# Kernel tuning notes

Measured on AMD Instinct MI355X. Metric: run time of the kernel, lower is better.

Reference implementation:

```python
import jax, jax.numpy as jnp
import numpy as np

B, S, H = 2, 2048, 1024
NH = 16
HD = H // NH

def setup_inputs() -> dict:
    key = jax.random.key(0)
    ks = jax.random.split(key, 9)
    s = 1.0 / np.sqrt(H)
    return {
        "hidden_state": jax.random.normal(ks[0], (B, S, H), dtype=jnp.float32),
        "Wq": jax.random.normal(ks[1], (H, H), dtype=jnp.float32) * s,
        "bq": jnp.zeros((H,), dtype=jnp.float32),
        "Wk": jax.random.normal(ks[2], (H, H), dtype=jnp.float32) * s,
        "bk": jnp.zeros((H,), dtype=jnp.float32),
        "Wv": jax.random.normal(ks[3], (H, H), dtype=jnp.float32) * s,
        "bv": jnp.zeros((H,), dtype=jnp.float32),
        "Wo": jax.random.normal(ks[4], (H, H), dtype=jnp.float32) * s,
        "bo": jnp.zeros((H,), dtype=jnp.float32),
    }

def reference(hidden_state, Wq, bq, Wk, bk, Wv, bv, Wo, bo):
    x = hidden_state  # [B,S,H]
    def split(t):
        return t.reshape(B, S, NH, HD).transpose(0, 2, 1, 3)  # [B,NH,S,HD]
    q = split(x @ Wq.T + bq)
    k = split(x @ Wk.T + bk)
    v = split(x @ Wv.T + bv)
    scale = 1.0 / jnp.sqrt(jnp.asarray(HD, dtype=x.dtype))
    scores = jnp.einsum('bhqd,bhkd->bhqk', q, k) * scale  # [B,NH,S,S]
    probs = jax.nn.softmax(scores, axis=-1)
    out = jnp.einsum('bhqk,bhkd->bhqd', probs, v)  # [B,NH,S,HD]
    out = out.transpose(0, 2, 1, 3).reshape(B, S, H)
    return out @ Wo.T + bo
```

## Files before the change

### kernel.cpp

```cpp
#include <hip/hip_runtime.h>


#define BD 2
#define SD 2048
#define HDIM 1024
#define NHD 16
#define HDD 64
#define NTOK 4096
#define QSCALE 0.1803368801111204f

typedef float f32x4 __attribute__((ext_vector_type(4)));
typedef _Float16 f16x8 __attribute__((ext_vector_type(8)));
typedef _Float16 f16x4 __attribute__((ext_vector_type(4)));
typedef __fp16 fp16x2 __attribute__((ext_vector_type(2)));

__device__ __forceinline__ f32x4 mfma_f16(f16x8 a, f16x8 b, f32x4 c) {
  return __builtin_amdgcn_mfma_f32_16x16x32_f16(a, b, c, 0, 0, 0);
}

__device__ __forceinline__ unsigned int pk2h(float lo, float hi) {
  fp16x2 v = __builtin_amdgcn_cvt_pkrtz(lo, hi);
  return __builtin_bit_cast(unsigned int, v);
}

__global__ void convert_kernel(const float* __restrict__ x,
                               const float* __restrict__ wq, const float* __restrict__ wk,
                               const float* __restrict__ wv, const float* __restrict__ wo,
                               _Float16* __restrict__ dst) {
  const int total4 = (8 * 1024 * 1024) / 4;
  for (int idx = blockIdx.x * blockDim.x + threadIdx.x; idx < total4;
       idx += gridDim.x * blockDim.x) {
    int e = idx * 4;
    const float* s;
    if (e < 4 * 1024 * 1024) {
      s = x + e;
    } else {
      int w = (e - 4 * 1024 * 1024) >> 20;
      int off = e & 1048575;
      s = (w == 0 ? wq : w == 1 ? wk : w == 2 ? wv : wo) + off;
    }
    float4 v = *(const float4*)s;
    f16x4 h;
    h[0] = (_Float16)v.x; h[1] = (_Float16)v.y;
    h[2] = (_Float16)v.z; h[3] = (_Float16)v.w;
    *(f16x4*)(dst + e) = h;
  }
}

__device__ __forceinline__ void gemm_mainloop(
    const _Float16* __restrict__ Ap, const _Float16* __restrict__ Bp,
    int i0, int j0, _Float16* As, _Float16* Bs, f32x4 acc[4][4]) {
  const int tid = threadIdx.x;
  const int wid = tid >> 6, lane = tid & 63;
  const int lr = lane & 15, lg = lane >> 4;
  const int wm = wid >> 1, wn = wid & 1;
  const int srow = lane >> 2;
  const int scol = (lane & 3) * 8;

  for (int k0 = 0; k0 < HDIM; k0 += 32) {
#pragma unroll
    for (int it = 0; it < 2; ++it) {
      int rb = (wid * 2 + it) * 16;
      const _Float16* ga = Ap + (size_t)(i0 + rb + srow) * HDIM + k0 + scol;
      const _Float16* gb = Bp + (size_t)(j0 + rb + srow) * HDIM + k0 + scol;
      __builtin_amdgcn_global_load_lds(
          (__attribute__((address_space(1))) void*)ga,
          (__attribute__((address_space(3))) void*)(As + (wid * 2 + it) * 512), 16, 0, 0);
      __builtin_amdgcn_global_load_lds(
          (__attribute__((address_space(1))) void*)gb,
          (__attribute__((address_space(3))) void*)(Bs + (wid * 2 + it) * 512), 16, 0, 0);
    }
    __syncthreads();
    f16x8 af[4], bf[4];
#pragma unroll
    for (int mt = 0; mt < 4; mt++)
      af[mt] = *(const f16x8*)(As + (wm * 64 + mt * 16 + lr) * 32 + lg * 8);
#pragma unroll
    for (int nt = 0; nt < 4; nt++)
      bf[nt] = *(const f16x8*)(Bs + (wn * 64 + nt * 16 + lr) * 32 + lg * 8);
#pragma unroll
    for (int mt = 0; mt < 4; mt++)
#pragma unroll
      for (int nt = 0; nt < 4; nt++)
        acc[mt][nt] = mfma_f16(af[mt], bf[nt], acc[mt][nt]);
    __syncthreads();
  }
}

__global__ __launch_bounds__(256) void gemm_qkv(
    const _Float16* __restrict__ xb,
    const _Float16* __restrict__ wqb, const _Float16* __restrict__ wkb,
    const _Float16* __restrict__ wvb,
    const float* __restrict__ bq, const float* __restrict__ bk,
    const float* __restrict__ bv,
    _Float16* __restrict__ Qo, _Float16* __restrict__ Ko, _Float16* __restrict__ Vt) {
  __shared__ __attribute__((aligned(16))) _Float16 As[128 * 32];
  __shared__ __attribute__((aligned(16))) _Float16 Bs[128 * 32];
  const int bx = blockIdx.x;
  const int mat = bx >> 8;
  const int sub = bx & 255;
  const _Float16 *Ap, *Bp;
  int i0, j0;
  if (mat < 2) {
    Ap = xb; Bp = (mat ? wkb : wqb);
    i0 = (sub >> 3) * 128;
    j0 = (sub & 7) * 128;
  } else {
    Ap = wvb; Bp = xb;
    i0 = (sub & 7) * 128;
    j0 = (sub >> 3) * 128;
  }
  f32x4 acc[4][4];
#pragma unroll
  for (int a = 0; a < 4; a++)
#pragma unroll
    for (int b = 0; b < 4; b++) acc[a][b] = (f32x4){0.f, 0.f, 0.f, 0.f};

  gemm_mainloop(Ap, Bp, i0, j0, As, Bs, acc);

  const int tid = threadIdx.x;
  const int wid = tid >> 6, lane = tid & 63;
  const int lr = lane & 15, lg = lane >> 4;
  const int wm = wid >> 1, wn = wid & 1;
  const float* bias = (mat == 0 ? bq : mat == 1 ? bk : bv);

#pragma unroll
  for (int mt = 0; mt < 4; mt++) {
#pragma unroll
    for (int nt = 0; nt < 4; nt++) {
      int i = i0 + wm * 64 + mt * 16 + 4 * lg;
      int j = j0 + wn * 64 + nt * 16 + lr;
      if (mat < 2) {
        float bj = bias[j];
        int h = j >> 6, d = j & 63;
        _Float16* dst = (mat ? Ko : Qo);
        float scl = (mat == 0) ? QSCALE : 1.0f;
#pragma unroll
        for (int r = 0; r < 4; r++) {
          int tok = i + r;
          int b = tok >> 11, s = tok & 2047;
          dst[(((size_t)(b * NHD + h)) * SD + s) * HDD + d] =
              (_Float16)((acc[mt][nt][r] + bj) * scl);
        }
      } else {
        int tok = j;
        int b = tok >> 11, s = tok & 2047;
#pragma unroll
        for (int r = 0; r < 4; r++) {
          int wr = i + r;
          int h = wr >> 6, d = wr & 63;
          Vt[((size_t)(b * NHD + h) * HDD + d) * SD + s] =
              (_Float16)(acc[mt][nt][r] + bias[wr]);
        }
      }
    }
  }
}

__global__ __launch_bounds__(256) void gemm_out(
    const _Float16* __restrict__ attn, const _Float16* __restrict__ wob,
    const float* __restrict__ bo, float* __restrict__ out) {
  __shared__ __attribute__((aligned(16))) _Float16 As[128 * 32];
  __shared__ __attribute__((aligned(16))) _Float16 Bs[128 * 32];
  const int sub = blockIdx.x;
  const int i0 = (sub >> 3) * 128, j0 = (sub & 7) * 128;
  f32x4 acc[4][4];
#pragma unroll
  for (int a = 0; a < 4; a++)
#pragma unroll
    for (int b = 0; b < 4; b++) acc[a][b] = (f32x4){0.f, 0.f, 0.f, 0.f};

  gemm_mainloop(attn, wob, i0, j0, As, Bs, acc);

  const int tid = threadIdx.x;
  const int wid = tid >> 6, lane = tid & 63;
  const int lr = lane & 15, lg = lane >> 4;
  const int wm = wid >> 1, wn = wid & 1;
#pragma unroll
  for (int mt = 0; mt < 4; mt++) {
#pragma unroll
    for (int nt = 0; nt < 4; nt++) {
      int i = i0 + wm * 64 + mt * 16 + 4 * lg;
      int j = j0 + wn * 64 + nt * 16 + lr;
      float bj = bo[j];
#pragma unroll
      for (int r = 0; r < 4; r++)
        out[(size_t)(i + r) * HDIM + j] = acc[mt][nt][r] + bj;
    }
  }
}

__global__ __launch_bounds__(512) void attn_kernel(
    const _Float16* __restrict__ Q, const _Float16* __restrict__ K,
    const _Float16* __restrict__ VT, _Float16* __restrict__ AO) {
  const int g = blockIdx.x;
  const int xcd = g & 7, idx = g >> 3;
  const int qb = idx & 15;
  const int bh = xcd * 4 + (idx >> 4);
  const int tid = threadIdx.x, wv = tid >> 6, lane = tid & 63;
  const int lr = lane & 15, lg = lane >> 4;
  const int q0 = qb * 128 + wv * 16;
  const _Float16* Qh = Q + (size_t)bh * SD * HDD;
  const _Float16* Kh = K + (size_t)bh * SD * HDD;
  const _Float16* Vh = VT + (size_t)bh * HDD * SD;

  __shared__ __attribute__((aligned(16))) _Float16 Ks[2][2][64][32];
  __shared__ __attribute__((aligned(16))) _Float16 Vs[2][2][64][32];

  const int krow = lane >> 2;
  const int kswz = (((lane & 3) ^ ((lane >> 3) & 3)) * 8);
  const int kkf = wv & 1, krb = (wv >> 1) * 16;

  const int m  = lane & 15;
  const int u  = m & 3;
  const int sg = m >> 2;
  const int r4 = lane >> 4;
  const int c2 = (r4 >> 1) & 1;
  const int keyoff_e = 16 * (u >> 1) + 4 * (sg ^ c2)       + 2 * (u & 1);
  const int keyoff_o = 16 * (u >> 1) + 4 * (sg ^ (c2 | 2)) + 2 * (u & 1);
  const _Float16* Vrow[2];
  Vrow[0] = Vh + (size_t)(wv * 8 + 0 + r4) * SD + keyoff_e;
  Vrow[1] = Vh + (size_t)(wv * 8 + 4 + r4) * SD + keyoff_o;

  auto stage = [&](int b, int kv0) {
    const _Float16* gk = Kh + (size_t)(kv0 + krb + krow) * HDD + kkf * 32 + kswz;
    __builtin_amdgcn_global_load_lds(
        (__attribute__((address_space(1))) void*)gk,
        (__attribute__((address_space(3))) void*)(&Ks[b][kkf][krb][0]), 16, 0, 0);
#pragma unroll
    for (int kf = 0; kf < 2; kf++)
#pragma unroll
      for (int i = 0; i < 2; i++) {
        const _Float16* gv = Vrow[i] + kv0 + kf * 32;
        __builtin_amdgcn_global_load_lds(
            (__attribute__((address_space(1))) void*)gv,
            (__attribute__((address_space(3))) void*)(&Vs[b][kf][wv * 8 + i * 4][0]), 4, 0, 0);
      }
  };

  const int fswz = (lg ^ ((lr >> 1) & 3)) * 8;

  f16x8 qf[2];
#pragma unroll
  for (int kf = 0; kf < 2; kf++)
    qf[kf] = *(const f16x8*)(Qh + (size_t)(q0 + lr) * HDD + kf * 32 + lg * 8);

  f32x4 acc[4];
#pragma unroll
  for (int i = 0; i < 4; i++) acc[i] = (f32x4){0.f, 0.f, 0.f, 0.f};
  float mrun = -1e30f;
  float ls0 = 0.f, ls1 = 0.f, ls2 = 0.f, ls3 = 0.f;

  stage(0, 0);
  int cur = 0;

  for (int t = 0; t < SD / 64; ++t) {
    asm volatile("s_waitcnt vmcnt(0)" ::: "memory");
    __builtin_amdgcn_s_barrier();
    stage(cur ^ 1, ((t + 1) & (SD / 64 - 1)) * 64);

    f32x4 sc[4];
#pragma unroll
    for (int nt = 0; nt < 4; nt++) sc[nt] = (f32x4){0.f, 0.f, 0.f, 0.f};
    __builtin_amdgcn_s_setprio(1);
#pragma unroll
    for (int nt = 0; nt < 4; nt++)
#pragma unroll
      for (int kf = 0; kf < 2; kf++) {
        f16x8 kfr = *(const f16x8*)&Ks[cur][kf][nt * 16 + lr][fswz];
        sc[nt] = mfma_f16(kfr, qf[kf], sc[nt]);
      }
    __builtin_amdgcn_s_setprio(0);

    float t0 = fmaxf(fmaxf(sc[0][0], sc[0][1]), sc[0][2]);
    float t1 = fmaxf(fmaxf(sc[0][3], sc[1][0]), sc[1][1]);
    float t2 = fmaxf(fmaxf(sc[1][2], sc[1][3]), sc[2][0]);
    float t3 = fmaxf(fmaxf(sc[2][1], sc[2][2]), sc[2][3]);
    float t4 = fmaxf(fmaxf(sc[3][0], sc[3][1]), sc[3][2]);
    float tm = fmaxf(fmaxf(fmaxf(t0, t1), fmaxf(t2, t3)), fmaxf(t4, sc[3][3]));
    tm = fmaxf(tm, __shfl_xor(tm, 16));
    tm = fmaxf(tm, __shfl_xor(tm, 32));

    if (__any(tm - mrun > 8.0f)) {
      float mn = fmaxf(mrun, tm);
      float fm = exp2f(mrun - mn);
      mrun = mn;
      ls0 *= fm; ls1 *= fm; ls2 *= fm; ls3 *= fm;
#pragma unroll
      for (int ntd = 0; ntd < 4; ntd++)
#pragma unroll
        for (int r = 0; r < 4; r++) acc[ntd][r] *= fm;
    }

    {
      float p0[4], p1[4];
#pragma unroll
      for (int r = 0; r < 4; r++) p0[r] = exp2f(sc[0][r] - mrun);
#pragma unroll
      for (int r = 0; r < 4; r++) p1[r] = exp2f(sc[1][r] - mrun);
      ls0 += (p0[0] + p0[1]) + (p0[2] + p0[3]);
      ls1 += (p1[0] + p1[1]) + (p1[2] + p1[3]);
      unsigned int pw[4];
      pw[0] = pk2h(p0[0], p0[1]); pw[1] = pk2h(p0[2], p0[3]);
      pw[2] = pk2h(p1[0], p1[1]); pw[3] = pk2h(p1[2], p1[3]);
      f16x8 pb = __builtin_bit_cast(f16x8, *(unsigned int(*)[4])pw);
      __builtin_amdgcn_s_setprio(1);
#pragma unroll
      for (int ntd = 0; ntd < 4; ntd++) {
        f16x8 vf = *(const f16x8*)&Vs[cur][0][ntd * 16 + lr][fswz];
        acc[ntd] = mfma_f16(vf, pb, acc[ntd]);
      }
      __builtin_amdgcn_s_setprio(0);
    }
    {
      float p0[4], p1[4];
#pragma unroll
      for (int r = 0; r < 4; r++) p0[r] = exp2f(sc[2][r] - mrun);
#pragma unroll
      for (int r = 0; r < 4; r++) p1[r] = exp2f(sc[3][r] - mrun);
      ls2 += (p0[0] + p0[1]) + (p0[2] + p0[3]);
      ls3 += (p1[0] + p1[1]) + (p1[2] + p1[3]);
      unsigned int pw[4];
      pw[0] = pk2h(p0[0], p0[1]); pw[1] = pk2h(p0[2], p0[3]);
      pw[2] = pk2h(p1[0], p1[1]); pw[3] = pk2h(p1[2], p1[3]);
      f16x8 pb = __builtin_bit_cast(f16x8, *(unsigned int(*)[4])pw);
      __builtin_amdgcn_s_setprio(1);
#pragma unroll
      for (int ntd = 0; ntd < 4; ntd++) {
        f16x8 vf = *(const f16x8*)&Vs[cur][1][ntd * 16 + lr][fswz];
        acc[ntd] = mfma_f16(vf, pb, acc[ntd]);
      }
      __builtin_amdgcn_s_setprio(0);
    }
    cur ^= 1;
  }

  float lsum = (ls0 + ls1) + (ls2 + ls3);
  lsum += __shfl_xor(lsum, 16);
  lsum += __shfl_xor(lsum, 32);
  float inv = 1.0f / lsum;

  const int b = bh >> 4, h = bh & 15;
  _Float16* aoRow = AO + (size_t)(b * SD + q0 + lr) * HDIM + h * 64;
#pragma unroll
  for (int ntd = 0; ntd < 4; ntd++) {
    f16x4 o;
#pragma unroll
    for (int r = 0; r < 4; r++) o[r] = (_Float16)(acc[ntd][r] * inv);
    *(f16x4*)(aoRow + ntd * 16 + 4 * lg) = o;
  }
}

extern "C" void kernel_launch(void* const* d_in, const int* in_sizes, int n_in,
                              void* d_out, int out_size, void* d_ws, size_t ws_size,
                              hipStream_t stream) {
  const float* x  = (const float*)d_in[0];
  const float* Wq = (const float*)d_in[1];
  const float* bq = (const float*)d_in[2];
  const float* Wk = (const float*)d_in[3];
  const float* bk = (const float*)d_in[4];
  const float* Wv = (const float*)d_in[5];
  const float* bv = (const float*)d_in[6];
  const float* Wo = (const float*)d_in[7];
  const float* bo = (const float*)d_in[8];
  float* out = (float*)d_out;

  _Float16* xb  = (_Float16*)d_ws;
  _Float16* wqb = xb + 4 * 1024 * 1024;
  _Float16* wkb = wqb + 1024 * 1024;
  _Float16* wvb = wkb + 1024 * 1024;
  _Float16* wob = wvb + 1024 * 1024;
  _Float16* Qb  = wob + 1024 * 1024;
  _Float16* Kb  = Qb + 4 * 1024 * 1024;
  _Float16* Vt  = Kb + 4 * 1024 * 1024;
  _Float16* AOb = Vt + 4 * 1024 * 1024;

  convert_kernel<<<dim3(1024), dim3(256), 0, stream>>>(x, Wq, Wk, Wv, Wo, xb);
  gemm_qkv<<<dim3(768), dim3(256), 0, stream>>>(xb, wqb, wkb, wvb, bq, bk, bv, Qb, Kb, Vt);
  attn_kernel<<<dim3(512), dim3(512), 0, stream>>>(Qb, Kb, Vt, AOb);
  gemm_out<<<dim3(256), dim3(256), 0, stream>>>(AOb, wob, bo, out);
}
```

Baseline: 139.4 us.

## Pre-permute V^T keys in projection epilogue and double KV tile to 128

The QKV projection now writes V^T with keys permuted within each 64-key group. This lets the attention kernel stage V with 16-byte direct-to-LDS loads using the same swizzle as K, instead of many 4-byte loads. The attention loop also processes 128 keys per iteration, which halves the number of barriers and max/rescale steps but doubles LDS use and score registers. The layout of V^T is coupled across both kernels, so the permutation must exactly match the MFMA operand order the attention kernel expects.

```diff
diff --git a/kernel.cpp b/kernel.cpp
--- a/kernel.cpp
+++ b/kernel.cpp
@@ -145,11 +145,14 @@
       } else {
         int tok = j;
         int b = tok >> 11, s = tok & 2047;
+        int w = s & 63;
+        int pos = (w & 32) + ((w & 12) << 1) + ((w & 16) >> 2) + (w & 3);
+        int sp = (s & ~63) | pos;
 #pragma unroll
         for (int r = 0; r < 4; r++) {
           int wr = i + r;
           int h = wr >> 6, d = wr & 63;
-          Vt[((size_t)(b * NHD + h) * HDD + d) * SD + s] =
+          Vt[((size_t)(b * NHD + h) * HDD + d) * SD + sp] =
               (_Float16)(acc[mt][nt][r] + bias[wr]);
         }
       }
@@ -204,38 +207,29 @@
   const _Float16* Kh = K + (size_t)bh * SD * HDD;
   const _Float16* Vh = VT + (size_t)bh * HDD * SD;
 
-  __shared__ __attribute__((aligned(16))) _Float16 Ks[2][2][64][32];
-  __shared__ __attribute__((aligned(16))) _Float16 Vs[2][2][64][32];
+  __shared__ __attribute__((aligned(16))) _Float16 Ks[2][2][128][32];
+  __shared__ __attribute__((aligned(16))) _Float16 Vs[2][4][64][32];
 
   const int krow = lane >> 2;
   const int kswz = (((lane & 3) ^ ((lane >> 3) & 3)) * 8);
-  const int kkf = wv & 1, krb = (wv >> 1) * 16;
-
-  const int m  = lane & 15;
-  const int u  = m & 3;
-  const int sg = m >> 2;
-  const int r4 = lane >> 4;
-  const int c2 = (r4 >> 1) & 1;
-  const int keyoff_e = 16 * (u >> 1) + 4 * (sg ^ c2)       + 2 * (u & 1);
-  const int keyoff_o = 16 * (u >> 1) + 4 * (sg ^ (c2 | 2)) + 2 * (u & 1);
-  const _Float16* Vrow[2];
-  Vrow[0] = Vh + (size_t)(wv * 8 + 0 + r4) * SD + keyoff_e;
-  Vrow[1] = Vh + (size_t)(wv * 8 + 4 + r4) * SD + keyoff_o;
+  const int kkf = wv & 1;
+  const int krb = (wv >> 1) * 16;
 
   auto stage = [&](int b, int kv0) {
-    const _Float16* gk = Kh + (size_t)(kv0 + krb + krow) * HDD + kkf * 32 + kswz;
-    __builtin_amdgcn_global_load_lds(
-        (__attribute__((address_space(1))) void*)gk,
-        (__attribute__((address_space(3))) void*)(&Ks[b][kkf][krb][0]), 16, 0, 0);
-#pragma unroll
-    for (int kf = 0; kf < 2; kf++)
-#pragma unroll
-      for (int i = 0; i < 2; i++) {
-        const _Float16* gv = Vrow[i] + kv0 + kf * 32;
-        __builtin_amdgcn_global_load_lds(
-            (__attribute__((address_space(1))) void*)gv,
-            (__attribute__((address_space(3))) void*)(&Vs[b][kf][wv * 8 + i * 4][0]), 4, 0, 0);
-      }
+#pragma unroll
+    for (int i = 0; i < 2; ++i) {
+      const _Float16* gk =
+          Kh + (size_t)(kv0 + i * 64 + krb + krow) * HDD + kkf * 32 + kswz;
+      __builtin_amdgcn_global_load_lds(
+          (__attribute__((address_space(1))) void*)gk,
+          (__attribute__((address_space(3))) void*)(&Ks[b][kkf][i * 64 + krb][0]), 16, 0, 0);
+      int kq = kkf * 2 + i;
+      const _Float16* gv =
+          Vh + (size_t)(krb + krow) * SD + kv0 + kq * 32 + kswz;
+      __builtin_amdgcn_global_load_lds(
+          (__attribute__((address_space(1))) void*)gv,
+          (__attribute__((address_space(3))) void*)(&Vs[b][kq][krb][0]), 16, 0, 0);
+    }
   };
 
   const int fswz = (lg ^ ((lr >> 1) & 3)) * 8;
@@ -254,30 +248,38 @@
   stage(0, 0);
   int cur = 0;
 
-  for (int t = 0; t < SD / 64; ++t) {
+  for (int t = 0; t < SD / 128; ++t) {
     asm volatile("s_waitcnt vmcnt(0)" ::: "memory");
     __builtin_amdgcn_s_barrier();
-    stage(cur ^ 1, ((t + 1) & (SD / 64 - 1)) * 64);
-
-    f32x4 sc[4];
-#pragma unroll
-    for (int nt = 0; nt < 4; nt++) sc[nt] = (f32x4){0.f, 0.f, 0.f, 0.f};
+    stage(cur ^ 1, ((t + 1) & (SD / 128 - 1)) * 128);
+
+    f32x4 sc[2][4];
+#pragma unroll
+    for (int h = 0; h < 2; h++)
+#pragma unroll
+      for (int nt = 0; nt < 4; nt++) sc[h][nt] = (f32x4){0.f, 0.f, 0.f, 0.f};
     __builtin_amdgcn_s_setprio(1);
 #pragma unroll
-    for (int nt = 0; nt < 4; nt++)
-#pragma unroll
-      for (int kf = 0; kf < 2; kf++) {
-        f16x8 kfr = *(const f16x8*)&Ks[cur][kf][nt * 16 + lr][fswz];
-        sc[nt] = mfma_f16(kfr, qf[kf], sc[nt]);
-      }
+    for (int h = 0; h < 2; h++)
+#pragma unroll
+      for (int nt = 0; nt < 4; nt++)
+#pragma unroll
+        for (int kf = 0; kf < 2; kf++) {
+          f16x8 kfr = *(const f16x8*)&Ks[cur][kf][h * 64 + nt * 16 + lr][fswz];
+          sc[h][nt] = mfma_f16(kfr, qf[kf], sc[h][nt]);
+        }
     __builtin_amdgcn_s_setprio(0);
 
-    float t0 = fmaxf(fmaxf(sc[0][0], sc[0][1]), sc[0][2]);
-    float t1 = fmaxf(fmaxf(sc[0][3], sc[1][0]), sc[1][1]);
-    float t2 = fmaxf(fmaxf(sc[1][2], sc[1][3]), sc[2][0]);
-    float t3 = fmaxf(fmaxf(sc[2][1], sc[2][2]), sc[2][3]);
-    float t4 = fmaxf(fmaxf(sc[3][0], sc[3][1]), sc[3][2]);
-    float tm = fmaxf(fmaxf(fmaxf(t0, t1), fmaxf(t2, t3)), fmaxf(t4, sc[3][3]));
+    float m0 = fmaxf(fmaxf(sc[0][0][0], sc[0][0][1]), fmaxf(sc[0][0][2], sc[0][0][3]));
+    float m1 = fmaxf(fmaxf(sc[0][1][0], sc[0][1][1]), fmaxf(sc[0][1][2], sc[0][1][3]));
+    float m2 = fmaxf(fmaxf(sc[0][2][0], sc[0][2][1]), fmaxf(sc[0][2][2], sc[0][2][3]));
+    float m3 = fmaxf(fmaxf(sc[0][3][0], sc[0][3][1]), fmaxf(sc[0][3][2], sc[0][3][3]));
+    float m4 = fmaxf(fmaxf(sc[1][0][0], sc[1][0][1]), fmaxf(sc[1][0][2], sc[1][0][3]));
+    float m5 = fmaxf(fmaxf(sc[1][1][0], sc[1][1][1]), fmaxf(sc[1][1][2], sc[1][1][3]));
+    float m6 = fmaxf(fmaxf(sc[1][2][0], sc[1][2][1]), fmaxf(sc[1][2][2], sc[1][2][3]));
+    float m7 = fmaxf(fmaxf(sc[1][3][0], sc[1][3][1]), fmaxf(sc[1][3][2], sc[1][3][3]));
+    float tm = fmaxf(fmaxf(fmaxf(m0, m1), fmaxf(m2, m3)),
+                     fmaxf(fmaxf(m4, m5), fmaxf(m6, m7)));
     tm = fmaxf(tm, __shfl_xor(tm, 16));
     tm = fmaxf(tm, __shfl_xor(tm, 32));
 
@@ -292,45 +294,31 @@
         for (int r = 0; r < 4; r++) acc[ntd][r] *= fm;
     }
 
-    {
-      float p0[4], p1[4];
-#pragma unroll
-      for (int r = 0; r < 4; r++) p0[r] = exp2f(sc[0][r] - mrun);
-#pragma unroll
-      for (int r = 0; r < 4; r++) p1[r] = exp2f(sc[1][r] - mrun);
-      ls0 += (p0[0] + p0[1]) + (p0[2] + p0[3]);
-      ls1 += (p1[0] + p1[1]) + (p1[2] + p1[3]);
-      unsigned int pw[4];
-      pw[0] = pk2h(p0[0], p0[1]); pw[1] = pk2h(p0[2], p0[3]);
-      pw[2] = pk2h(p1[0], p1[1]); pw[3] = pk2h(p1[2], p1[3]);
-      f16x8 pb = __builtin_bit_cast(f16x8, *(unsigned int(*)[4])pw);
-      __builtin_amdgcn_s_setprio(1);
-#pragma unroll
-      for (int ntd = 0; ntd < 4; ntd++) {
-        f16x8 vf = *(const f16x8*)&Vs[cur][0][ntd * 16 + lr][fswz];
-        acc[ntd] = mfma_f16(vf, pb, acc[ntd]);
+#pragma unroll
+    for (int h = 0; h < 2; h++) {
+#pragma unroll
+      for (int kf = 0; kf < 2; kf++) {
+        float p0[4], p1[4];
+#pragma unroll
+        for (int r = 0; r < 4; r++) p0[r] = exp2f(sc[h][2 * kf][r] - mrun);
+#pragma unroll
+        for (int r = 0; r < 4; r++) p1[r] = exp2f(sc[h][2 * kf + 1][r] - mrun);
+        float s01 = (p0[0] + p0[1]) + (p0[2] + p0[3]);
+        float s23 = (p1[0] + p1[1]) + (p1[2] + p1[3]);
+        if (h == 0) { if (kf == 0) { ls0 += s01; ls1 += s23; } else { ls2 += s01; ls3 += s23; } }
+        else        { if (kf == 0) { ls0 += s01; ls1 += s23; } else { ls2 += s01; ls3 += s23; } }
+        unsigned int pw[4];
+        pw[0] = pk2h(p0[0], p0[1]); pw[1] = pk2h(p0[2], p0[3]);
+        pw[2] = pk2h(p1[0], p1[1]); pw[3] = pk2h(p1[2], p1[3]);
+        f16x8 pb = __builtin_bit_cast(f16x8, *(unsigned int(*)[4])pw);
+        __builtin_amdgcn_s_setprio(1);
+#pragma unroll
+        for (int ntd = 0; ntd < 4; ntd++) {
+          f16x8 vf = *(const f16x8*)&Vs[cur][h * 2 + kf][ntd * 16 + lr][fswz];
+          acc[ntd] = mfma_f16(vf, pb, acc[ntd]);
+        }
+        __builtin_amdgcn_s_setprio(0);
       }
-      __builtin_amdgcn_s_setprio(0);
-    }
-    {
-      float p0[4], p1[4];
-#pragma unroll
-      for (int r = 0; r < 4; r++) p0[r] = exp2f(sc[2][r] - mrun);
-#pragma unroll
-      for (int r = 0; r < 4; r++) p1[r] = exp2f(sc[3][r] - mrun);
-      ls2 += (p0[0] + p0[1]) + (p0[2] + p0[3]);
-      ls3 += (p1[0] + p1[1]) + (p1[2] + p1[3]);
-      unsigned int pw[4];
-      pw[0] = pk2h(p0[0], p0[1]); pw[1] = pk2h(p0[2], p0[3]);
-      pw[2] = pk2h(p1[0], p1[1]); pw[3] = pk2h(p1[2], p1[3]);
-      f16x8 pb = __builtin_bit_cast(f16x8, *(unsigned int(*)[4])pw);
-      __builtin_amdgcn_s_setprio(1);
-#pragma unroll
-      for (int ntd = 0; ntd < 4; ntd++) {
-        f16x8 vf = *(const f16x8*)&Vs[cur][1][ntd * 16 + lr][fswz];
-        acc[ntd] = mfma_f16(vf, pb, acc[ntd]);
-      }
-      __builtin_amdgcn_s_setprio(0);
     }
     cur ^= 1;
   }
```

Result: faster. 135.7 us (-2.7%).
